# Optimization experiments

Hardware: AMD Instinct MI355X
Metric: run time of the kernel (lower is better)

Reference implementation:

```python
import jax, jax.numpy as jnp
import numpy as np

L, B, D = 50, 1024, 512      # memory slots, batch, d_model
H, DK = 4, 512               # heads, per-head dim (d_k = d_model in this module)
HOP = 3


def setup_inputs() -> dict:
    key = jax.random.key(0)
    ks = jax.random.split(key, 16)
    s = lambda i, shape: jax.random.normal(ks[i], shape, jnp.float32) * 0.02
    return dict(
        momery=jax.random.normal(ks[0], (L, B, D), jnp.float32),
        hid=jax.random.normal(ks[1], (B, D), jnp.float32),
        text_polarity=jax.random.normal(ks[2], (B,), jnp.float32),
        attribute_polarity=jax.random.normal(ks[3], (B,), jnp.float32),
        w=jnp.array(0.5, jnp.float32),
        p_w1=s(4, (D, D)), p_b1=jnp.zeros((D,), jnp.float32),
        p_w2=s(5, (D, D)), p_b2=jnp.zeros((D,), jnp.float32),
        wq=s(6, (D, H * DK)), bq=jnp.zeros((H * DK,), jnp.float32),
        wk=s(7, (D, H * DK)), bk=jnp.zeros((H * DK,), jnp.float32),
        wv=s(8, (D, H * DK)), bv=jnp.zeros((H * DK,), jnp.float32),
        wo=s(9, (H * DK, D)), bo=jnp.zeros((D,), jnp.float32),
    )


def reference(momery, hid, text_polarity, attribute_polarity, w,
              p_w1, p_b1, p_w2, p_b2, wq, bq, wk, bk, wv, bv, wo, bo):
    # k, v depend only on hid (attinkv = hid every hop/slot) -> hoist out of hop loop
    k = (hid @ wk + bk).reshape(B, H, DK)   # [B,H,DK]
    v = (hid @ wv + bv).reshape(B, H, DK)   # [B,H,DK]
    inv_sqrt_dk = jnp.float32(1.0 / np.sqrt(DK))
    for _ in range(HOP):
        # projection MLP over all slots at once (replaces per-slot loop)
        mid = jax.nn.relu(momery @ p_w1 + p_b1) @ p_w2 + p_b2          # [L,B,D]
        q = (mid @ wq + bq).reshape(L, B, H, DK)                        # [L,B,H,DK]
        # single key per query (nk=1): scores [L,B,H,1], softmax -> ones
        scores = (jnp.einsum('lbhd,bhd->lbh', q, k) * inv_sqrt_dk)[..., None]
        att = jax.nn.softmax(scores, axis=-1)                           # [L,B,H,1]
        out = att * v                                                   # [L,B,H,DK]
        temp = out.reshape(L, B, H * DK) @ wo + bo                      # [L,B,D]
        momery = momery + w * temp
    return momery
```

## Files before the change

### kernel.cpp

```cpp
#include <hip/hip_runtime.h>
#include <hip/hip_bf16.h>

typedef short short8 __attribute__((ext_vector_type(8)));
typedef float f4 __attribute__((ext_vector_type(4)));

__device__ __forceinline__ short f2bfs(float f) {
    __hip_bfloat16 h = __float2bfloat16(f);
    return __builtin_bit_cast(short, h);
}

__device__ __forceinline__ unsigned packbf2(float a, float b, float s) {
    unsigned lo = (unsigned short)f2bfs(s * a);
    unsigned hi = (unsigned short)f2bfs(s * b);
    return (hi << 16) | lo;
}

__device__ __forceinline__ float4 add4(float4 m, float4 t) {
    float4 o; o.x = m.x + t.x; o.y = m.y + t.y; o.z = m.z + t.z; o.w = m.w + t.w;
    return o;
}

__global__ __launch_bounds__(512) void prepW(const float* __restrict__ wv,
                                             const float* __restrict__ wo,
                                             const float* __restrict__ bv,
                                             const float* __restrict__ w,
                                             short* __restrict__ WsT,
                                             float* __restrict__ b2p) {
    constexpr int K = 2048, N = 512, NT = 32;
    const int tid = threadIdx.x;
    const int bx  = blockIdx.x;

    if (bx >= 64) {
        const int jb  = bx - 64;
        const int col = tid;
        const float* pv = bv + jb * 512;
        const float* pw = wo + (size_t)(jb * 512) * N + col;
        float s = 0.f;
#pragma unroll 8
        for (int j = 0; j < 512; ++j) s += pv[j] * pw[(size_t)j * N];
        b2p[jb * 512 + col] = s;
        return;
    }

    __shared__ float red[64][65];

    const int col0 = (bx & 7) * 64;
    const int row0 = (bx >> 3) * 64;
    const int lane = tid & 63;
    const int wave = tid >> 6;
    const int half = wave >> 2;
    const int wq   = wave & 3;
    const int mq = wq >> 1, nq = wq & 1;
    const int ln = lane & 15, q = lane >> 4;
    const int k0 = half * 1024;

    const int rowA0 = row0 + mq * 32 + ln;
    const int rowA1 = rowA0 + 16;
    const int colB0 = col0 + nq * 32 + ln;
    const int colB1 = colB0 + 16;

    const float* pa0 = wv + (size_t)rowA0 * K + k0 + q * 8;
    const float* pa1 = wv + (size_t)rowA1 * K + k0 + q * 8;
    const float* pb  = wo + (size_t)(k0 + q * 8) * N;

    float4 a00 = *(const float4*)pa0, a01 = *(const float4*)(pa0 + 4);
    float4 a10 = *(const float4*)pa1, a11 = *(const float4*)(pa1 + 4);
    float b0r[8], b1r[8];
#pragma unroll
    for (int j = 0; j < 8; ++j) {
        b0r[j] = pb[(size_t)j * N + colB0];
        b1r[j] = pb[(size_t)j * N + colB1];
    }

    f4 acc00 = {0,0,0,0}, acc01 = {0,0,0,0}, acc10 = {0,0,0,0}, acc11 = {0,0,0,0};

    for (int t = 0; t < NT; ++t) {
        short8 af0, af1, bf0, bf1;
        af0[0]=f2bfs(a00.x); af0[1]=f2bfs(a00.y); af0[2]=f2bfs(a00.z); af0[3]=f2bfs(a00.w);
        af0[4]=f2bfs(a01.x); af0[5]=f2bfs(a01.y); af0[6]=f2bfs(a01.z); af0[7]=f2bfs(a01.w);
        af1[0]=f2bfs(a10.x); af1[1]=f2bfs(a10.y); af1[2]=f2bfs(a10.z); af1[3]=f2bfs(a10.w);
        af1[4]=f2bfs(a11.x); af1[5]=f2bfs(a11.y); af1[6]=f2bfs(a11.z); af1[7]=f2bfs(a11.w);
#pragma unroll
        for (int j = 0; j < 8; ++j) { bf0[j] = f2bfs(b0r[j]); bf1[j] = f2bfs(b1r[j]); }

        if (t + 1 < NT) {
            pa0 += 32; pa1 += 32; pb += (size_t)32 * N;
            a00 = *(const float4*)pa0; a01 = *(const float4*)(pa0 + 4);
            a10 = *(const float4*)pa1; a11 = *(const float4*)(pa1 + 4);
#pragma unroll
            for (int j = 0; j < 8; ++j) {
                b0r[j] = pb[(size_t)j * N + colB0];
                b1r[j] = pb[(size_t)j * N + colB1];
            }
        }
        acc00 = __builtin_amdgcn_mfma_f32_16x16x32_bf16(af0, bf0, acc00, 0, 0, 0);
        acc01 = __builtin_amdgcn_mfma_f32_16x16x32_bf16(af0, bf1, acc01, 0, 0, 0);
        acc10 = __builtin_amdgcn_mfma_f32_16x16x32_bf16(af1, bf0, acc10, 0, 0, 0);
        acc11 = __builtin_amdgcn_mfma_f32_16x16x32_bf16(af1, bf1, acc11, 0, 0, 0);
    }

    const int lr0 = mq * 32 + q * 4;
    const int lc0 = nq * 32 + ln;

    if (half == 1) {
#pragma unroll
        for (int r = 0; r < 4; ++r) {
            red[lr0 + r][lc0]           = acc00[r];
            red[lr0 + r][lc0 + 16]      = acc01[r];
            red[lr0 + 16 + r][lc0]      = acc10[r];
            red[lr0 + 16 + r][lc0 + 16] = acc11[r];
        }
    }
    __syncthreads();
    if (half == 0) {
        const float wsc = 3.0f * w[0];
#pragma unroll
        for (int r = 0; r < 4; ++r) {
            acc00[r] += red[lr0 + r][lc0];
            acc01[r] += red[lr0 + r][lc0 + 16];
            acc10[r] += red[lr0 + 16 + r][lc0];
            acc11[r] += red[lr0 + 16 + r][lc0 + 16];
        }
        short* p0 = WsT + (size_t)(col0 + lc0) * 512 + row0 + lr0;
        short* p1 = WsT + (size_t)(col0 + lc0 + 16) * 512 + row0 + lr0;
        *(unsigned*)(p0)      = packbf2(acc00[0], acc00[1], wsc);
        *(unsigned*)(p0 + 2)  = packbf2(acc00[2], acc00[3], wsc);
        *(unsigned*)(p0 + 16) = packbf2(acc10[0], acc10[1], wsc);
        *(unsigned*)(p0 + 18) = packbf2(acc10[2], acc10[3], wsc);
        *(unsigned*)(p1)      = packbf2(acc01[0], acc01[1], wsc);
        *(unsigned*)(p1 + 2)  = packbf2(acc01[2], acc01[3], wsc);
        *(unsigned*)(p1 + 16) = packbf2(acc11[0], acc11[1], wsc);
        *(unsigned*)(p1 + 18) = packbf2(acc11[2], acc11[3], wsc);
    }
}

__global__ __launch_bounds__(256) void fusedTB(const float* __restrict__ hid,
                                               const short* __restrict__ WsT,
                                               const float* __restrict__ b2p,
                                               const float* __restrict__ bo,
                                               const float* __restrict__ w,
                                               const float* __restrict__ mem,
                                               float* __restrict__ out) {
    constexpr int KD = 512, NT = 16;
    constexpr size_t LS = 1024 * 512 / 4;
    __shared__ float tT[16][64];

    const int tid  = threadIdx.x;
    const int b0   = blockIdx.x * 16;
    const int c0   = blockIdx.y * 64;
    const int lane = tid & 63;
    const int wave = tid >> 6;
    const int ln = lane & 15, q = lane >> 4;
    const int row = b0 + ln;
    const int col = c0 + wave * 16 + ln;

    const int sr  = tid >> 4;
    const int sc4 = tid & 15;
    const size_t sbase = (size_t)(b0 + sr) * 512 + c0 + sc4 * 4;
    const float4* mp = (const float4*)(mem + sbase);
    float4*       op = (float4*)(out + sbase);
    float4 m0 = mp[0], m1 = mp[LS], m2 = mp[2 * LS], m3 = mp[3 * LS], m4 = mp[4 * LS];

    const float* pa  = hid + (size_t)row * KD + q * 8;
    const short* pbw = WsT + (size_t)col * KD + q * 8;

    float4 a0 = *(const float4*)pa, a1 = *(const float4*)(pa + 4);
    short8 bf = *(const short8*)pbw;
    f4 acc = {0, 0, 0, 0};

    for (int t = 0; t < NT; ++t) {
        short8 af;
        af[0]=f2bfs(a0.x); af[1]=f2bfs(a0.y); af[2]=f2bfs(a0.z); af[3]=f2bfs(a0.w);
        af[4]=f2bfs(a1.x); af[5]=f2bfs(a1.y); af[6]=f2bfs(a1.z); af[7]=f2bfs(a1.w);
        short8 bc = bf;
        if (t + 1 < NT) {
            pa += 32; pbw += 32;
            a0 = *(const float4*)pa; a1 = *(const float4*)(pa + 4);
            bf = *(const short8*)pbw;
        }
        acc = __builtin_amdgcn_mfma_f32_16x16x32_bf16(af, bc, acc, 0, 0, 0);
    }

    const float wsc  = 3.0f * w[0];
    const float bias = wsc * (b2p[col] + b2p[512 + col] + b2p[1024 + col] +
                              b2p[1536 + col] + bo[col]);
#pragma unroll
    for (int r = 0; r < 4; ++r) tT[q * 4 + r][wave * 16 + ln] = acc[r] + bias;
    __syncthreads();

    const float4 tv = *(const float4*)&tT[sr][sc4 * 4];

    op[0]      = add4(m0, tv);
    op[LS]     = add4(m1, tv);
    op[2 * LS] = add4(m2, tv);
    op[3 * LS] = add4(m3, tv);
    op[4 * LS] = add4(m4, tv);
    mp += 5 * LS; op += 5 * LS;
    for (int c = 1; c < 10; ++c) {
        m0 = mp[0]; m1 = mp[LS]; m2 = mp[2 * LS]; m3 = mp[3 * LS]; m4 = mp[4 * LS];
        op[0]      = add4(m0, tv);
        op[LS]     = add4(m1, tv);
        op[2 * LS] = add4(m2, tv);
        op[3 * LS] = add4(m3, tv);
        op[4 * LS] = add4(m4, tv);
        mp += 5 * LS; op += 5 * LS;
    }
}

extern "C" void kernel_launch(void* const* d_in, const int* in_sizes, int n_in,
                              void* d_out, int out_size, void* d_ws, size_t ws_size,
                              hipStream_t stream) {
    const float* momery = (const float*)d_in[0];
    const float* hid    = (const float*)d_in[1];
    const float* w      = (const float*)d_in[4];
    const float* wv     = (const float*)d_in[13];
    const float* bv     = (const float*)d_in[14];
    const float* wo     = (const float*)d_in[15];
    const float* bo     = (const float*)d_in[16];
    float* out = (float*)d_out;

    short* WsT = (short*)d_ws;
    float* b2p = (float*)(WsT + 262144);

    prepW<<<dim3(68), 512, 0, stream>>>(wv, wo, bv, w, WsT, b2p);

    fusedTB<<<dim3(64, 8), 256, 0, stream>>>(hid, WsT, b2p, bo, w, momery, out);
}
```

Measured before the change: 275.8 us.

## Reassociate V·O projection and split broadcast into a separate high-occupancy streaming kernel

Instead of first folding Wv@Wo into one weight and fusing hid@Ws with the memory broadcast, the code now converts and transposes wv, wo and hid to bf16. It computes U = hid@Wv + bv, then hid-side T = U@Wo + bo, split along K into two partial outputs, and runs a separate 5120-block broadcast kernel using nontemporal loads and stores. The goal is to remove the poorly parallelised weight-prep stage and the low-occupancy fused broadcast that streams the 50-slot memory. The cost is more GEMM FLOPs, an extra fp32 intermediate round trip and two additional launches.

```diff
diff --git a/kernel.cpp b/kernel.cpp
--- a/kernel.cpp
+++ b/kernel.cpp
@@ -9,94 +9,142 @@
     return __builtin_bit_cast(short, h);
 }
 
-__device__ __forceinline__ unsigned packbf2(float a, float b, float s) {
-    unsigned lo = (unsigned short)f2bfs(s * a);
-    unsigned hi = (unsigned short)f2bfs(s * b);
-    return (hi << 16) | lo;
-}
-
-__device__ __forceinline__ float4 add4(float4 m, float4 t) {
-    float4 o; o.x = m.x + t.x; o.y = m.y + t.y; o.z = m.z + t.z; o.w = m.w + t.w;
-    return o;
-}
-
-__global__ __launch_bounds__(512) void prepW(const float* __restrict__ wv,
-                                             const float* __restrict__ wo,
+#define MFMA(a, b, c) __builtin_amdgcn_mfma_f32_16x16x32_bf16(a, b, c, 0, 0, 0)
+
+__global__ __launch_bounds__(256) void prep(const float* __restrict__ wv,
+                                            const float* __restrict__ wo,
+                                            const float* __restrict__ hid,
+                                            short* __restrict__ wvT,
+                                            short* __restrict__ woT,
+                                            short* __restrict__ hidB) {
+    const int bx  = blockIdx.x;
+    const int tid = threadIdx.x;
+
+    if (bx >= 512) {
+        const int idx = (bx - 512) * 2048 + tid * 8;
+        const float4 a = *(const float4*)(hid + idx);
+        const float4 b = *(const float4*)(hid + idx + 4);
+        short8 o;
+        o[0]=f2bfs(a.x); o[1]=f2bfs(a.y); o[2]=f2bfs(a.z); o[3]=f2bfs(a.w);
+        o[4]=f2bfs(b.x); o[5]=f2bfs(b.y); o[6]=f2bfs(b.z); o[7]=f2bfs(b.w);
+        *(short8*)(hidB + idx) = o;
+        return;
+    }
+
+    const float* src; short* dst; int N, M, tm, tn;
+    if (bx < 256) { src = wv; dst = wvT; M = 512;  N = 2048; tm = bx & 7;         tn = bx >> 3; }
+    else          { src = wo; dst = woT; M = 2048; N = 512;  tm = (bx - 256) >> 3; tn = (bx - 256) & 7; }
+
+    __shared__ short tile[64][65];
+    const int r  = tid >> 4;
+    const int c4 = tid & 15;
+#pragma unroll
+    for (int rr = 0; rr < 64; rr += 16) {
+        const float4 v = *(const float4*)(src + (size_t)(tm * 64 + r + rr) * N + tn * 64 + c4 * 4);
+        tile[c4 * 4 + 0][r + rr] = f2bfs(v.x);
+        tile[c4 * 4 + 1][r + rr] = f2bfs(v.y);
+        tile[c4 * 4 + 2][r + rr] = f2bfs(v.z);
+        tile[c4 * 4 + 3][r + rr] = f2bfs(v.w);
+    }
+    __syncthreads();
+    const int d  = tid >> 2;
+    const int ch = tid & 3;
+    short8 o0, o1;
+#pragma unroll
+    for (int j = 0; j < 8; ++j) { o0[j] = tile[d][ch * 16 + j]; o1[j] = tile[d][ch * 16 + 8 + j]; }
+    short* p = dst + (size_t)(tn * 64 + d) * M + tm * 64 + ch * 16;
+    *(short8*)p       = o0;
+    *(short8*)(p + 8) = o1;
+}
+
+__global__ __launch_bounds__(256) void gemmU(const short* __restrict__ hidB,
+                                             const short* __restrict__ wvT,
                                              const float* __restrict__ bv,
-                                             const float* __restrict__ w,
-                                             short* __restrict__ WsT,
-                                             float* __restrict__ b2p) {
-    constexpr int K = 2048, N = 512, NT = 32;
-    const int tid = threadIdx.x;
-    const int bx  = blockIdx.x;
-
-    if (bx >= 64) {
-        const int jb  = bx - 64;
-        const int col = tid;
-        const float* pv = bv + jb * 512;
-        const float* pw = wo + (size_t)(jb * 512) * N + col;
-        float s = 0.f;
-#pragma unroll 8
-        for (int j = 0; j < 512; ++j) s += pv[j] * pw[(size_t)j * N];
-        b2p[jb * 512 + col] = s;
-        return;
-    }
-
+                                             float* __restrict__ U) {
+    constexpr int K = 512, N = 2048, NT = 16;
+    const int tid  = threadIdx.x;
+    const int col0 = blockIdx.x * 64;
+    const int row0 = blockIdx.y * 64;
+    const int lane = tid & 63, wave = tid >> 6;
+    const int mq = wave >> 1, nq = wave & 1;
+    const int ln = lane & 15, q = lane >> 4;
+
+    const short* pa0 = hidB + (size_t)(row0 + mq * 32 + ln) * K + q * 8;
+    const short* pa1 = pa0 + 16 * K;
+    const short* pb0 = wvT + (size_t)(col0 + nq * 32 + ln) * K + q * 8;
+    const short* pb1 = pb0 + 16 * K;
+
+    short8 af0 = *(const short8*)pa0, af1 = *(const short8*)pa1;
+    short8 bf0 = *(const short8*)pb0, bf1 = *(const short8*)pb1;
+    f4 acc00 = {0,0,0,0}, acc01 = {0,0,0,0}, acc10 = {0,0,0,0}, acc11 = {0,0,0,0};
+
+    for (int t = 0; t < NT; ++t) {
+        short8 a0 = af0, a1 = af1, b0 = bf0, b1 = bf1;
+        if (t + 1 < NT) {
+            pa0 += 32; pa1 += 32; pb0 += 32; pb1 += 32;
+            af0 = *(const short8*)pa0; af1 = *(const short8*)pa1;
+            bf0 = *(const short8*)pb0; bf1 = *(const short8*)pb1;
+        }
+        acc00 = MFMA(a0, b0, acc00); acc01 = MFMA(a0, b1, acc01);
+        acc10 = MFMA(a1, b0, acc10); acc11 = MFMA(a1, b1, acc11);
+    }
+
+    const int r0 = row0 + mq * 32 + q * 4;
+    const int c0 = col0 + nq * 32 + ln;
+    const float bv0 = bv[c0], bv1 = bv[c0 + 16];
+#pragma unroll
+    for (int r = 0; r < 4; ++r) {
+        U[(size_t)(r0 + r) * N + c0]           = acc00[r] + bv0;
+        U[(size_t)(r0 + r) * N + c0 + 16]      = acc01[r] + bv1;
+        U[(size_t)(r0 + 16 + r) * N + c0]      = acc10[r] + bv0;
+        U[(size_t)(r0 + 16 + r) * N + c0 + 16] = acc11[r] + bv1;
+    }
+}
+
+__global__ __launch_bounds__(512) void gemmT(const float* __restrict__ U,
+                                             const short* __restrict__ woT,
+                                             const float* __restrict__ bo,
+                                             float* __restrict__ t0,
+                                             float* __restrict__ t1) {
+    constexpr int K = 2048, N = 512, NT = 16;
     __shared__ float red[64][65];
 
-    const int col0 = (bx & 7) * 64;
-    const int row0 = (bx >> 3) * 64;
-    const int lane = tid & 63;
-    const int wave = tid >> 6;
-    const int half = wave >> 2;
-    const int wq   = wave & 3;
+    const int tid  = threadIdx.x;
+    const int col0 = blockIdx.x * 64;
+    const int row0 = blockIdx.y * 64;
+    const int z    = blockIdx.z;
+    const int lane = tid & 63, wave = tid >> 6;
+    const int half = wave >> 2, wq = wave & 3;
     const int mq = wq >> 1, nq = wq & 1;
     const int ln = lane & 15, q = lane >> 4;
-    const int k0 = half * 1024;
-
-    const int rowA0 = row0 + mq * 32 + ln;
-    const int rowA1 = rowA0 + 16;
-    const int colB0 = col0 + nq * 32 + ln;
-    const int colB1 = colB0 + 16;
-
-    const float* pa0 = wv + (size_t)rowA0 * K + k0 + q * 8;
-    const float* pa1 = wv + (size_t)rowA1 * K + k0 + q * 8;
-    const float* pb  = wo + (size_t)(k0 + q * 8) * N;
+    const int k0 = z * 1024 + half * 512;
+
+    const float* pa0 = U + (size_t)(row0 + mq * 32 + ln) * K + k0 + q * 8;
+    const float* pa1 = pa0 + (size_t)16 * K;
+    const short* pb0 = woT + (size_t)(col0 + nq * 32 + ln) * K + k0 + q * 8;
+    const short* pb1 = pb0 + (size_t)16 * K;
 
     float4 a00 = *(const float4*)pa0, a01 = *(const float4*)(pa0 + 4);
     float4 a10 = *(const float4*)pa1, a11 = *(const float4*)(pa1 + 4);
-    float b0r[8], b1r[8];
-#pragma unroll
-    for (int j = 0; j < 8; ++j) {
-        b0r[j] = pb[(size_t)j * N + colB0];
-        b1r[j] = pb[(size_t)j * N + colB1];
-    }
+    short8 bf0 = *(const short8*)pb0, bf1 = *(const short8*)pb1;
 
     f4 acc00 = {0,0,0,0}, acc01 = {0,0,0,0}, acc10 = {0,0,0,0}, acc11 = {0,0,0,0};
 
     for (int t = 0; t < NT; ++t) {
-        short8 af0, af1, bf0, bf1;
+        short8 af0, af1;
         af0[0]=f2bfs(a00.x); af0[1]=f2bfs(a00.y); af0[2]=f2bfs(a00.z); af0[3]=f2bfs(a00.w);
         af0[4]=f2bfs(a01.x); af0[5]=f2bfs(a01.y); af0[6]=f2bfs(a01.z); af0[7]=f2bfs(a01.w);
         af1[0]=f2bfs(a10.x); af1[1]=f2bfs(a10.y); af1[2]=f2bfs(a10.z); af1[3]=f2bfs(a10.w);
         af1[4]=f2bfs(a11.x); af1[5]=f2bfs(a11.y); af1[6]=f2bfs(a11.z); af1[7]=f2bfs(a11.w);
-#pragma unroll
-        for (int j = 0; j < 8; ++j) { bf0[j] = f2bfs(b0r[j]); bf1[j] = f2bfs(b1r[j]); }
-
+        short8 b0 = bf0, b1 = bf1;
         if (t + 1 < NT) {
-            pa0 += 32; pa1 += 32; pb += (size_t)32 * N;
+            pa0 += 32; pa1 += 32; pb0 += 32; pb1 += 32;
             a00 = *(const float4*)pa0; a01 = *(const float4*)(pa0 + 4);
             a10 = *(const float4*)pa1; a11 = *(const float4*)(pa1 + 4);
-#pragma unroll
-            for (int j = 0; j < 8; ++j) {
-                b0r[j] = pb[(size_t)j * N + colB0];
-                b1r[j] = pb[(size_t)j * N + colB1];
-            }
-        }
-        acc00 = __builtin_amdgcn_mfma_f32_16x16x32_bf16(af0, bf0, acc00, 0, 0, 0);
-        acc01 = __builtin_amdgcn_mfma_f32_16x16x32_bf16(af0, bf1, acc01, 0, 0, 0);
-        acc10 = __builtin_amdgcn_mfma_f32_16x16x32_bf16(af1, bf0, acc10, 0, 0, 0);
-        acc11 = __builtin_amdgcn_mfma_f32_16x16x32_bf16(af1, bf1, acc11, 0, 0, 0);
+            bf0 = *(const short8*)pb0; bf1 = *(const short8*)pb1;
+        }
+        acc00 = MFMA(af0, b0, acc00); acc01 = MFMA(af0, b1, acc01);
+        acc10 = MFMA(af1, b0, acc10); acc11 = MFMA(af1, b1, acc11);
     }
 
     const int lr0 = mq * 32 + q * 4;
@@ -113,97 +161,40 @@
     }
     __syncthreads();
     if (half == 0) {
-        const float wsc = 3.0f * w[0];
+        float bb0 = 0.f, bb1 = 0.f;
+        if (z == 0) { bb0 = bo[col0 + lc0]; bb1 = bo[col0 + lc0 + 16]; }
+        float* C = z ? t1 : t0;
+        const int r0 = row0 + lr0;
+        const int c0 = col0 + lc0;
 #pragma unroll
         for (int r = 0; r < 4; ++r) {
-            acc00[r] += red[lr0 + r][lc0];
-            acc01[r] += red[lr0 + r][lc0 + 16];
-            acc10[r] += red[lr0 + 16 + r][lc0];
-            acc11[r] += red[lr0 + 16 + r][lc0 + 16];
-        }
-        short* p0 = WsT + (size_t)(col0 + lc0) * 512 + row0 + lr0;
-        short* p1 = WsT + (size_t)(col0 + lc0 + 16) * 512 + row0 + lr0;
-        *(unsigned*)(p0)      = packbf2(acc00[0], acc00[1], wsc);
-        *(unsigned*)(p0 + 2)  = packbf2(acc00[2], acc00[3], wsc);
-        *(unsigned*)(p0 + 16) = packbf2(acc10[0], acc10[1], wsc);
-        *(unsigned*)(p0 + 18) = packbf2(acc10[2], acc10[3], wsc);
-        *(unsigned*)(p1)      = packbf2(acc01[0], acc01[1], wsc);
-        *(unsigned*)(p1 + 2)  = packbf2(acc01[2], acc01[3], wsc);
-        *(unsigned*)(p1 + 16) = packbf2(acc11[0], acc11[1], wsc);
-        *(unsigned*)(p1 + 18) = packbf2(acc11[2], acc11[3], wsc);
-    }
-}
-
-__global__ __launch_bounds__(256) void fusedTB(const float* __restrict__ hid,
-                                               const short* __restrict__ WsT,
-                                               const float* __restrict__ b2p,
-                                               const float* __restrict__ bo,
-                                               const float* __restrict__ w,
-                                               const float* __restrict__ mem,
-                                               float* __restrict__ out) {
-    constexpr int KD = 512, NT = 16;
-    constexpr size_t LS = 1024 * 512 / 4;
-    __shared__ float tT[16][64];
-
-    const int tid  = threadIdx.x;
-    const int b0   = blockIdx.x * 16;
-    const int c0   = blockIdx.y * 64;
-    const int lane = tid & 63;
-    const int wave = tid >> 6;
-    const int ln = lane & 15, q = lane >> 4;
-    const int row = b0 + ln;
-    const int col = c0 + wave * 16 + ln;
-
-    const int sr  = tid >> 4;
-    const int sc4 = tid & 15;
-    const size_t sbase = (size_t)(b0 + sr) * 512 + c0 + sc4 * 4;
-    const float4* mp = (const float4*)(mem + sbase);
-    float4*       op = (float4*)(out + sbase);
-    float4 m0 = mp[0], m1 = mp[LS], m2 = mp[2 * LS], m3 = mp[3 * LS], m4 = mp[4 * LS];
-
-    const float* pa  = hid + (size_t)row * KD + q * 8;
-    const short* pbw = WsT + (size_t)col * KD + q * 8;
-
-    float4 a0 = *(const float4*)pa, a1 = *(const float4*)(pa + 4);
-    short8 bf = *(const short8*)pbw;
-    f4 acc = {0, 0, 0, 0};
-
-    for (int t = 0; t < NT; ++t) {
-        short8 af;
-        af[0]=f2bfs(a0.x); af[1]=f2bfs(a0.y); af[2]=f2bfs(a0.z); af[3]=f2bfs(a0.w);
-        af[4]=f2bfs(a1.x); af[5]=f2bfs(a1.y); af[6]=f2bfs(a1.z); af[7]=f2bfs(a1.w);
-        short8 bc = bf;
-        if (t + 1 < NT) {
-            pa += 32; pbw += 32;
-            a0 = *(const float4*)pa; a1 = *(const float4*)(pa + 4);
-            bf = *(const short8*)pbw;
-        }
-        acc = __builtin_amdgcn_mfma_f32_16x16x32_bf16(af, bc, acc, 0, 0, 0);
-    }
-
-    const float wsc  = 3.0f * w[0];
-    const float bias = wsc * (b2p[col] + b2p[512 + col] + b2p[1024 + col] +
-                              b2p[1536 + col] + bo[col]);
-#pragma unroll
-    for (int r = 0; r < 4; ++r) tT[q * 4 + r][wave * 16 + ln] = acc[r] + bias;
-    __syncthreads();
-
-    const float4 tv = *(const float4*)&tT[sr][sc4 * 4];
-
-    op[0]      = add4(m0, tv);
-    op[LS]     = add4(m1, tv);
-    op[2 * LS] = add4(m2, tv);
-    op[3 * LS] = add4(m3, tv);
-    op[4 * LS] = add4(m4, tv);
-    mp += 5 * LS; op += 5 * LS;
-    for (int c = 1; c < 10; ++c) {
-        m0 = mp[0]; m1 = mp[LS]; m2 = mp[2 * LS]; m3 = mp[3 * LS]; m4 = mp[4 * LS];
-        op[0]      = add4(m0, tv);
-        op[LS]     = add4(m1, tv);
-        op[2 * LS] = add4(m2, tv);
-        op[3 * LS] = add4(m3, tv);
-        op[4 * LS] = add4(m4, tv);
-        mp += 5 * LS; op += 5 * LS;
+            C[(size_t)(r0 + r) * N + c0]           = acc00[r] + red[lr0 + r][lc0] + bb0;
+            C[(size_t)(r0 + r) * N + c0 + 16]      = acc01[r] + red[lr0 + r][lc0 + 16] + bb1;
+            C[(size_t)(r0 + 16 + r) * N + c0]      = acc10[r] + red[lr0 + 16 + r][lc0] + bb0;
+            C[(size_t)(r0 + 16 + r) * N + c0 + 16] = acc11[r] + red[lr0 + 16 + r][lc0 + 16] + bb1;
+        }
+    }
+}
+
+__global__ __launch_bounds__(256) void bcast(const float* __restrict__ mem,
+                                             const float* __restrict__ t0,
+                                             const float* __restrict__ t1,
+                                             const float* __restrict__ w,
+                                             float* __restrict__ out) {
+    constexpr int P = 131072;
+    const int id  = blockIdx.x * 256 + threadIdx.x;
+    const int bd4 = id & (P - 1);
+    const int grp = id >> 17;
+    const float s = 3.0f * w[0];
+    const f4 a = ((const f4*)t0)[bd4];
+    const f4 b = ((const f4*)t1)[bd4];
+    const f4 tv = s * (a + b);
+    const f4* mp = (const f4*)mem + (size_t)grp * 5 * P + bd4;
+    f4*       op = (f4*)out       + (size_t)grp * 5 * P + bd4;
+#pragma unroll
+    for (int j = 0; j < 5; ++j) {
+        f4 m = __builtin_nontemporal_load(mp + (size_t)j * P);
+        __builtin_nontemporal_store(m + tv, op + (size_t)j * P);
     }
 }
 
@@ -219,10 +210,15 @@
     const float* bo     = (const float*)d_in[16];
     float* out = (float*)d_out;
 
-    short* WsT = (short*)d_ws;
-    float* b2p = (float*)(WsT + 262144);
-
-    prepW<<<dim3(68), 512, 0, stream>>>(wv, wo, bv, w, WsT, b2p);
-
-    fusedTB<<<dim3(64, 8), 256, 0, stream>>>(hid, WsT, b2p, bo, w, momery, out);
-}
+    short* wvT  = (short*)d_ws;
+    short* woT  = wvT + 2048 * 512;
+    short* hidB = woT + 2048 * 512;
+    float* U    = (float*)(hidB + 1024 * 512);
+    float* t0   = U + 1024 * 2048;
+    float* t1   = t0 + 1024 * 512;
+
+    prep<<<768, 256, 0, stream>>>(wv, wo, hid, wvT, woT, hidB);
+    gemmU<<<dim3(32, 16), 256, 0, stream>>>(hidB, wvT, bv, U);
+    gemmT<<<dim3(8, 16, 2), 512, 0, stream>>>(U, woT, bo, t0, t1);
+    bcast<<<5120, 256, 0, stream>>>(momery, t0, t1, w, out);
+}
```

New measurement: 260.3 us. 5.6% less time.

## Split fused GEMM+broadcast into three kernels with finer weight-product tiling

Applied to the files above, without the earlier changes.

The weight-product kernel now uses 256 blocks of 32x32 tiles with a 4-way split-K reduction, replacing 64 blocks with a 2-way split. The hid GEMM writes the update tensor to workspace, and a separate, fully parallel broadcast kernel adds it to all 50 memory slots using nontemporal loads and stores. The aim is more parallelism and better bandwidth on the dominant memory-bound broadcast, which was previously serialized over slots in only 512 blocks. The cost is an extra kernel launch and a round trip of the temporary update tensor through global memory.

```diff
diff --git a/kernel.cpp b/kernel.cpp
--- a/kernel.cpp
+++ b/kernel.cpp
@@ -15,52 +15,43 @@
     return (hi << 16) | lo;
 }
 
-__device__ __forceinline__ float4 add4(float4 m, float4 t) {
-    float4 o; o.x = m.x + t.x; o.y = m.y + t.y; o.z = m.z + t.z; o.w = m.w + t.w;
-    return o;
-}
+#define MFMA(a, b, c) __builtin_amdgcn_mfma_f32_16x16x32_bf16(a, b, c, 0, 0, 0)
 
-__global__ __launch_bounds__(512) void prepW(const float* __restrict__ wv,
+__global__ __launch_bounds__(256) void gemmW(const float* __restrict__ wv,
                                              const float* __restrict__ wo,
                                              const float* __restrict__ bv,
                                              const float* __restrict__ w,
                                              short* __restrict__ WsT,
                                              float* __restrict__ b2p) {
-    constexpr int K = 2048, N = 512, NT = 32;
+    constexpr int K = 2048, N = 512, NT = 16;
     const int tid = threadIdx.x;
     const int bx  = blockIdx.x;
 
-    if (bx >= 64) {
-        const int jb  = bx - 64;
-        const int col = tid;
+    if (bx >= 256) {
+        const int jb = bx - 256;
         const float* pv = bv + jb * 512;
-        const float* pw = wo + (size_t)(jb * 512) * N + col;
-        float s = 0.f;
+#pragma unroll
+        for (int cc = 0; cc < 2; ++cc) {
+            const int c = tid + cc * 256;
+            const float* pw = wo + (size_t)(jb * 512) * N + c;
+            float s = 0.f;
 #pragma unroll 8
-        for (int j = 0; j < 512; ++j) s += pv[j] * pw[(size_t)j * N];
-        b2p[jb * 512 + col] = s;
+            for (int j = 0; j < 512; ++j) s += pv[j] * pw[(size_t)j * N];
+            b2p[jb * 512 + c] = s;
+        }
         return;
     }
 
-    __shared__ float red[64][65];
+    __shared__ float red[4][32][33];
 
-    const int col0 = (bx & 7) * 64;
-    const int row0 = (bx >> 3) * 64;
-    const int lane = tid & 63;
-    const int wave = tid >> 6;
-    const int half = wave >> 2;
-    const int wq   = wave & 3;
-    const int mq = wq >> 1, nq = wq & 1;
+    const int row0 = (bx >> 4) * 32;
+    const int col0 = (bx & 15) * 32;
+    const int lane = tid & 63, wave = tid >> 6;
     const int ln = lane & 15, q = lane >> 4;
-    const int k0 = half * 1024;
+    const int k0 = wave * 512;
 
-    const int rowA0 = row0 + mq * 32 + ln;
-    const int rowA1 = rowA0 + 16;
-    const int colB0 = col0 + nq * 32 + ln;
-    const int colB1 = colB0 + 16;
-
-    const float* pa0 = wv + (size_t)rowA0 * K + k0 + q * 8;
-    const float* pa1 = wv + (size_t)rowA1 * K + k0 + q * 8;
+    const float* pa0 = wv + (size_t)(row0 + ln) * K + k0 + q * 8;
+    const float* pa1 = pa0 + (size_t)16 * K;
     const float* pb  = wo + (size_t)(k0 + q * 8) * N;
 
     float4 a00 = *(const float4*)pa0, a01 = *(const float4*)(pa0 + 4);
@@ -68,8 +59,8 @@
     float b0r[8], b1r[8];
 #pragma unroll
     for (int j = 0; j < 8; ++j) {
-        b0r[j] = pb[(size_t)j * N + colB0];
-        b1r[j] = pb[(size_t)j * N + colB1];
+        b0r[j] = pb[(size_t)j * N + col0 + ln];
+        b1r[j] = pb[(size_t)j * N + col0 + 16 + ln];
     }
 
     f4 acc00 = {0,0,0,0}, acc01 = {0,0,0,0}, acc10 = {0,0,0,0}, acc11 = {0,0,0,0};
@@ -89,121 +80,100 @@
             a10 = *(const float4*)pa1; a11 = *(const float4*)(pa1 + 4);
 #pragma unroll
             for (int j = 0; j < 8; ++j) {
-                b0r[j] = pb[(size_t)j * N + colB0];
-                b1r[j] = pb[(size_t)j * N + colB1];
+                b0r[j] = pb[(size_t)j * N + col0 + ln];
+                b1r[j] = pb[(size_t)j * N + col0 + 16 + ln];
             }
         }
-        acc00 = __builtin_amdgcn_mfma_f32_16x16x32_bf16(af0, bf0, acc00, 0, 0, 0);
-        acc01 = __builtin_amdgcn_mfma_f32_16x16x32_bf16(af0, bf1, acc01, 0, 0, 0);
-        acc10 = __builtin_amdgcn_mfma_f32_16x16x32_bf16(af1, bf0, acc10, 0, 0, 0);
-        acc11 = __builtin_amdgcn_mfma_f32_16x16x32_bf16(af1, bf1, acc11, 0, 0, 0);
+        acc00 = MFMA(af0, bf0, acc00); acc01 = MFMA(af0, bf1, acc01);
+        acc10 = MFMA(af1, bf0, acc10); acc11 = MFMA(af1, bf1, acc11);
     }
 
-    const int lr0 = mq * 32 + q * 4;
-    const int lc0 = nq * 32 + ln;
-
-    if (half == 1) {
 #pragma unroll
-        for (int r = 0; r < 4; ++r) {
-            red[lr0 + r][lc0]           = acc00[r];
-            red[lr0 + r][lc0 + 16]      = acc01[r];
-            red[lr0 + 16 + r][lc0]      = acc10[r];
-            red[lr0 + 16 + r][lc0 + 16] = acc11[r];
-        }
+    for (int r = 0; r < 4; ++r) {
+        red[wave][q * 4 + r][ln]           = acc00[r];
+        red[wave][q * 4 + r][ln + 16]      = acc01[r];
+        red[wave][16 + q * 4 + r][ln]      = acc10[r];
+        red[wave][16 + q * 4 + r][ln + 16] = acc11[r];
     }
     __syncthreads();
-    if (half == 0) {
-        const float wsc = 3.0f * w[0];
-#pragma unroll
-        for (int r = 0; r < 4; ++r) {
-            acc00[r] += red[lr0 + r][lc0];
-            acc01[r] += red[lr0 + r][lc0 + 16];
-            acc10[r] += red[lr0 + 16 + r][lc0];
-            acc11[r] += red[lr0 + 16 + r][lc0 + 16];
-        }
-        short* p0 = WsT + (size_t)(col0 + lc0) * 512 + row0 + lr0;
-        short* p1 = WsT + (size_t)(col0 + lc0 + 16) * 512 + row0 + lr0;
-        *(unsigned*)(p0)      = packbf2(acc00[0], acc00[1], wsc);
-        *(unsigned*)(p0 + 2)  = packbf2(acc00[2], acc00[3], wsc);
-        *(unsigned*)(p0 + 16) = packbf2(acc10[0], acc10[1], wsc);
-        *(unsigned*)(p0 + 18) = packbf2(acc10[2], acc10[3], wsc);
-        *(unsigned*)(p1)      = packbf2(acc01[0], acc01[1], wsc);
-        *(unsigned*)(p1 + 2)  = packbf2(acc01[2], acc01[3], wsc);
-        *(unsigned*)(p1 + 16) = packbf2(acc11[0], acc11[1], wsc);
-        *(unsigned*)(p1 + 18) = packbf2(acc11[2], acc11[3], wsc);
-    }
+
+    const float wsc = 3.0f * w[0];
+    const int n  = tid >> 3;
+    const int d0 = (tid & 7) * 4;
+    float s0 = red[0][d0][n]     + red[1][d0][n]     + red[2][d0][n]     + red[3][d0][n];
+    float s1 = red[0][d0 + 1][n] + red[1][d0 + 1][n] + red[2][d0 + 1][n] + red[3][d0 + 1][n];
+    float s2 = red[0][d0 + 2][n] + red[1][d0 + 2][n] + red[2][d0 + 2][n] + red[3][d0 + 2][n];
+    float s3 = red[0][d0 + 3][n] + red[1][d0 + 3][n] + red[2][d0 + 3][n] + red[3][d0 + 3][n];
+    short* p = WsT + (size_t)(col0 + n) * 512 + row0 + d0;
+    *(unsigned*)p       = packbf2(s0, s1, wsc);
+    *(unsigned*)(p + 2) = packbf2(s2, s3, wsc);
 }
 
-__global__ __launch_bounds__(256) void fusedTB(const float* __restrict__ hid,
-                                               const short* __restrict__ WsT,
-                                               const float* __restrict__ b2p,
-                                               const float* __restrict__ bo,
-                                               const float* __restrict__ w,
-                                               const float* __restrict__ mem,
-                                               float* __restrict__ out) {
-    constexpr int KD = 512, NT = 16;
-    constexpr size_t LS = 1024 * 512 / 4;
-    __shared__ float tT[16][64];
+__global__ __launch_bounds__(256) void gemmT(const float* __restrict__ hid,
+                                             const short* __restrict__ WsT,
+                                             const float* __restrict__ b2p,
+                                             const float* __restrict__ bo,
+                                             const float* __restrict__ w,
+                                             float* __restrict__ t) {
+    constexpr int K = 512, N = 512, NT = 16;
+    const int tid  = threadIdx.x;
+    const int col0 = blockIdx.x * 64;
+    const int row0 = blockIdx.y * 32;
+    const int lane = tid & 63, wave = tid >> 6;
+    const int ln = lane & 15, q = lane >> 4;
+    const int col = col0 + wave * 16 + ln;
 
-    const int tid  = threadIdx.x;
-    const int b0   = blockIdx.x * 16;
-    const int c0   = blockIdx.y * 64;
-    const int lane = tid & 63;
-    const int wave = tid >> 6;
-    const int ln = lane & 15, q = lane >> 4;
-    const int row = b0 + ln;
-    const int col = c0 + wave * 16 + ln;
+    const float* pa0 = hid + (size_t)(row0 + ln) * K + q * 8;
+    const float* pa1 = pa0 + (size_t)16 * K;
+    const short* pb  = WsT + (size_t)col * K + q * 8;
 
-    const int sr  = tid >> 4;
-    const int sc4 = tid & 15;
-    const size_t sbase = (size_t)(b0 + sr) * 512 + c0 + sc4 * 4;
-    const float4* mp = (const float4*)(mem + sbase);
-    float4*       op = (float4*)(out + sbase);
-    float4 m0 = mp[0], m1 = mp[LS], m2 = mp[2 * LS], m3 = mp[3 * LS], m4 = mp[4 * LS];
+    float4 a00 = *(const float4*)pa0, a01 = *(const float4*)(pa0 + 4);
+    float4 a10 = *(const float4*)pa1, a11 = *(const float4*)(pa1 + 4);
+    short8 bf = *(const short8*)pb;
 
-    const float* pa  = hid + (size_t)row * KD + q * 8;
-    const short* pbw = WsT + (size_t)col * KD + q * 8;
+    f4 acc0 = {0,0,0,0}, acc1 = {0,0,0,0};
 
-    float4 a0 = *(const float4*)pa, a1 = *(const float4*)(pa + 4);
-    short8 bf = *(const short8*)pbw;
-    f4 acc = {0, 0, 0, 0};
-
-    for (int t = 0; t < NT; ++t) {
-        short8 af;
-        af[0]=f2bfs(a0.x); af[1]=f2bfs(a0.y); af[2]=f2bfs(a0.z); af[3]=f2bfs(a0.w);
-        af[4]=f2bfs(a1.x); af[5]=f2bfs(a1.y); af[6]=f2bfs(a1.z); af[7]=f2bfs(a1.w);
-        short8 bc = bf;
-        if (t + 1 < NT) {
-            pa += 32; pbw += 32;
-            a0 = *(const float4*)pa; a1 = *(const float4*)(pa + 4);
-            bf = *(const short8*)pbw;
+    for (int tt = 0; tt < NT; ++tt) {
+        short8 af0, af1;
+        af0[0]=f2bfs(a00.x); af0[1]=f2bfs(a00.y); af0[2]=f2bfs(a00.z); af0[3]=f2bfs(a00.w);
+        af0[4]=f2bfs(a01.x); af0[5]=f2bfs(a01.y); af0[6]=f2bfs(a01.z); af0[7]=f2bfs(a01.w);
+        af1[0]=f2bfs(a10.x); af1[1]=f2bfs(a10.y); af1[2]=f2bfs(a10.z); af1[3]=f2bfs(a10.w);
+        af1[4]=f2bfs(a11.x); af1[5]=f2bfs(a11.y); af1[6]=f2bfs(a11.z); af1[7]=f2bfs(a11.w);
+        short8 b = bf;
+        if (tt + 1 < NT) {
+            pa0 += 32; pa1 += 32; pb += 32;
+            a00 = *(const float4*)pa0; a01 = *(const float4*)(pa0 + 4);
+            a10 = *(const float4*)pa1; a11 = *(const float4*)(pa1 + 4);
+            bf = *(const short8*)pb;
         }
-        acc = __builtin_amdgcn_mfma_f32_16x16x32_bf16(af, bc, acc, 0, 0, 0);
+        acc0 = MFMA(af0, b, acc0);
+        acc1 = MFMA(af1, b, acc1);
     }
 
     const float wsc  = 3.0f * w[0];
     const float bias = wsc * (b2p[col] + b2p[512 + col] + b2p[1024 + col] +
                               b2p[1536 + col] + bo[col]);
 #pragma unroll
-    for (int r = 0; r < 4; ++r) tT[q * 4 + r][wave * 16 + ln] = acc[r] + bias;
-    __syncthreads();
+    for (int r = 0; r < 4; ++r) {
+        t[(size_t)(row0 + q * 4 + r) * N + col]      = acc0[r] + bias;
+        t[(size_t)(row0 + 16 + q * 4 + r) * N + col] = acc1[r] + bias;
+    }
+}
 
-    const float4 tv = *(const float4*)&tT[sr][sc4 * 4];
-
-    op[0]      = add4(m0, tv);
-    op[LS]     = add4(m1, tv);
-    op[2 * LS] = add4(m2, tv);
-    op[3 * LS] = add4(m3, tv);
-    op[4 * LS] = add4(m4, tv);
-    mp += 5 * LS; op += 5 * LS;
-    for (int c = 1; c < 10; ++c) {
-        m0 = mp[0]; m1 = mp[LS]; m2 = mp[2 * LS]; m3 = mp[3 * LS]; m4 = mp[4 * LS];
-        op[0]      = add4(m0, tv);
-        op[LS]     = add4(m1, tv);
-        op[2 * LS] = add4(m2, tv);
-        op[3 * LS] = add4(m3, tv);
-        op[4 * LS] = add4(m4, tv);
-        mp += 5 * LS; op += 5 * LS;
+__global__ __launch_bounds__(256) void bcast(const float* __restrict__ mem,
+                                             const float* __restrict__ t,
+                                             float* __restrict__ out) {
+    constexpr int P = 131072;
+    const int id  = blockIdx.x * 256 + threadIdx.x;
+    const int bd4 = id & (P - 1);
+    const int grp = id >> 17;
+    const f4 tv = ((const f4*)t)[bd4];
+    const f4* mp = (const f4*)mem + (size_t)grp * 5 * P + bd4;
+    f4*       op = (f4*)out       + (size_t)grp * 5 * P + bd4;
+#pragma unroll
+    for (int j = 0; j < 5; ++j) {
+        f4 m = __builtin_nontemporal_load(mp + (size_t)j * P);
+        __builtin_nontemporal_store(m + tv, op + (size_t)j * P);
     }
 }
 
@@ -221,8 +191,9 @@
 
     short* WsT = (short*)d_ws;
     float* b2p = (float*)(WsT + 262144);
+    float* t   = b2p + 2048;
 
-    prepW<<<dim3(68), 512, 0, stream>>>(wv, wo, bv, w, WsT, b2p);
-
-    fusedTB<<<dim3(64, 8), 256, 0, stream>>>(hid, WsT, b2p, bo, w, momery, out);
+    gemmW<<<260, 256, 0, stream>>>(wv, wo, bv, w, WsT, b2p);
+    gemmT<<<dim3(8, 32), 256, 0, stream>>>(hid, WsT, b2p, bo, w, t);
+    bcast<<<5120, 256, 0, stream>>>(momery, t, out);
 }
```

Result: no change. 280.4 us (+1.7%).
